# Kernel optimization log

Hardware: AMD Instinct MI355X
Metric: run time of the kernel (lower is better)

The kernel has to match this reference:

```python
import jax, jax.numpy as jnp
import numpy as np

N = 50000   # nodes
E = 500000  # edges
D = 128     # enc_dim == Hout
INIT_W = 0.1


def _lin_w(k, din, dout):
    return jax.random.normal(k, (dout, din), jnp.float32) * INIT_W


def setup_inputs() -> dict:
    key = jax.random.key(0)
    ks = jax.random.split(key, 16)
    inp = {
        "x": jax.random.normal(ks[0], (N, D), jnp.float32),
        "src": jax.random.randint(ks[1], (E,), 0, N),
        "dst": jax.random.randint(ks[2], (E,), 0, N),
        # encoders (Linear enc_dim -> enc_dim)
        "WencK": _lin_w(ks[3], D, D), "bencK": jnp.zeros((D,), jnp.float32),
        "WencP1": _lin_w(ks[4], D, D), "bencP1": jnp.zeros((D,), jnp.float32),
        "WencP2": _lin_w(ks[5], D, D), "bencP2": jnp.zeros((D,), jnp.float32),
        # Kfun: Linear-Tanh-Linear-ReLU-Linear
        "K0W": _lin_w(ks[6], D, D), "K0b": jnp.zeros((D,), jnp.float32),
        "K1W": _lin_w(ks[7], D, D), "K1b": jnp.zeros((D,), jnp.float32),
        "K2W": _lin_w(ks[8], D, D), "K2b": jnp.zeros((D,), jnp.float32),
        # Ufun: Linear-Tanh-Linear-ReLU-Linear
        "U0W": _lin_w(ks[9], D, D), "U0b": jnp.zeros((D,), jnp.float32),
        "U1W": _lin_w(ks[10], D, D), "U1b": jnp.zeros((D,), jnp.float32),
        "U2W": _lin_w(ks[11], D, D), "U2b": jnp.zeros((D,), jnp.float32),
    }
    return inp


def _mlp3(h, W0, b0, W1, b1, W2, b2):
    h = jnp.tanh(h @ W0.T + b0)
    h = jax.nn.relu(h @ W1.T + b1)
    return h @ W2.T + b2


def reference(x, src, dst,
              WencK, bencK, WencP1, bencP1, WencP2, bencP2,
              K0W, K0b, K1W, K1b, K2W, K2b,
              U0W, U0b, U1W, U1b, U2W, U2b):
    # getK: encode nodes, copy_u + sum to dst, node MLP
    h1 = x @ WencK.T + bencK                                   # [N, D]
    h1_agg = jax.ops.segment_sum(h1[src], dst, num_segments=N)  # [N, D]
    Knode = _mlp3(h1_agg, K0W, K0b, K1W, K1b, K2W, K2b)         # [N, D]
    # getU: u_add_v on encoded features, edge MLP
    p1 = x @ WencP1.T + bencP1
    p2 = x @ WencP2.T + bencP2
    Eedge = _mlp3(p1[src] + p2[dst], U0W, U0b, U1W, U1b, U2W, U2b)  # [E, D]
    # getH: u_mul_e + sum to dst
    Enew = jax.ops.segment_sum(Knode[src] * Eedge, dst, num_segments=N)  # [N, D]
    return jnp.sum(Enew)
```

## Files before the change

### kernel.cpp

```cpp
#include <hip/hip_runtime.h>
#include <hip/hip_bf16.h>
#include <math.h>

#define NN 50000
#define NE 500000
#define DD 128
#define STR 136
#define NSCAN (2 * NN)
#define SCAN_BLK ((NSCAN + 1023) / 1024)
#define HIST_BLK ((NE + 255) / 256)
#define CVT_BLK  ((NN * DD + 4095) / 4096)
#define PRECONV_BLK ((7 * 2048 + 1023) / 1024)
#define ENC_BLK  ((NN + 127) / 128)
#define TSCALE 2.885390081777927f

typedef __attribute__((ext_vector_type(8))) short short8;
typedef __attribute__((ext_vector_type(4))) float floatx4;

__device__ __forceinline__ float bf2f(unsigned short u) {
    unsigned v = ((unsigned)u) << 16;
    float f;
    __builtin_memcpy(&f, &v, 4);
    return f;
}
__device__ __forceinline__ unsigned short f2bf(float f) {
    unsigned x;
    __builtin_memcpy(&x, &f, 4);
    x += 0x7FFF + ((x >> 16) & 1);
    return (unsigned short)(x >> 16);
}
__device__ __forceinline__ float fast_tanh(float x) {
    float t = __builtin_amdgcn_exp2f(x * TSCALE);
    return 1.f - 2.f * __builtin_amdgcn_rcpf(t + 1.f);
}
__device__ __forceinline__ float fast_tanh_pre(float u) {
    float t = __builtin_amdgcn_exp2f(u);
    return 1.f - 2.f * __builtin_amdgcn_rcpf(t + 1.f);
}

__global__ __launch_bounds__(256) void k1_kernel(
    const int* __restrict__ src, const int* __restrict__ dst,
    int* __restrict__ cnt_dst, int* __restrict__ cnt_src,
    int* __restrict__ rank_d, int* __restrict__ rank_s,
    const float* __restrict__ x, unsigned short* __restrict__ xbf,
    const float* __restrict__ U0W, const float* __restrict__ WencP1,
    const float* __restrict__ WencP2, const float* __restrict__ K0W,
    const float* __restrict__ WencK,
    const float* __restrict__ bp1, const float* __restrict__ bp2,
    const float* __restrict__ U0b, const float* __restrict__ bk,
    const float* __restrict__ U2b,
    float* __restrict__ comp, float* __restrict__ bvecs)
{
    __shared__ float Bs[DD * DD];
    int blk = blockIdx.x;
    int t = threadIdx.x;

    if (blk < HIST_BLK) {
        int e = blk * 256 + t;
        if (e < NE) {
            rank_d[e] = atomicAdd(&cnt_dst[dst[e]], 1);
            rank_s[e] = atomicAdd(&cnt_src[src[e]], 1);
        }
        return;
    }
    if (blk < HIST_BLK + CVT_BLK) {
        int base = (blk - HIST_BLK) * 4096;
        #pragma unroll
        for (int j = 0; j < 4; ++j) {
            int idx = base + (j * 256 + t) * 4;
            if (idx < NN * DD) {
                float4 f = *(const float4*)&x[idx];
                ushort4 v4;
                v4.x = f2bf(f.x); v4.y = f2bf(f.y);
                v4.z = f2bf(f.z); v4.w = f2bf(f.w);
                *(ushort4*)&xbf[idx] = v4;
            }
        }
        return;
    }

    int b = blk - (HIST_BLK + CVT_BLK);
    if (b == 6) {
        if (t < 128) {
            float s1 = 0.f, s2 = 0.f;
            for (int k = 0; k < DD; ++k) {
                s1 += U0W[t * DD + k] * (bp1[k] + bp2[k]);
                s2 += K0W[t * DD + k] * bk[k];
            }
            bvecs[t] = (s1 + U0b[t]) * TSCALE;
            bvecs[128 + t] = s2;
            int f = (t & 64) + 16 * (t & 3) + ((t & 63) >> 2);
            bvecs[256 + t] = U2b[f];
        }
        return;
    }
    int mat = b >> 1, half = b & 1;
    const float* A = (mat == 2) ? K0W : U0W;
    const float* B = (mat == 0) ? WencP1 : (mat == 1) ? WencP2 : WencK;
    float scl = (mat == 2) ? 1.f : TSCALE;
    float* C = comp + (size_t)mat * DD * DD;
    for (int i = 0; i < 64; ++i)
        Bs[i * 256 + t] = B[i * 256 + t];
    __syncthreads();
    int row = half * 64 + (t >> 2);
    int j0 = (t & 3) * 32;
    float acc[32];
    #pragma unroll
    for (int jj = 0; jj < 32; ++jj) acc[jj] = 0.f;
    for (int k = 0; k < DD; ++k) {
        float a = A[row * DD + k];
        #pragma unroll
        for (int jj = 0; jj < 32; ++jj)
            acc[jj] += a * Bs[k * DD + j0 + jj];
    }
    #pragma unroll
    for (int jj = 0; jj < 32; ++jj) C[row * DD + j0 + jj] = acc[jj] * scl;
}

__global__ __launch_bounds__(1024) void k2_kernel(
    const float* __restrict__ comp, const float* __restrict__ K1W,
    const float* __restrict__ K2W, const float* __restrict__ U2W,
    const float* __restrict__ U1W, unsigned short* __restrict__ wfrag,
    const int* __restrict__ cnt, int* __restrict__ base, int* __restrict__ bsum)
{
    int t = threadIdx.x;
    if (blockIdx.x < PRECONV_BLK) {
        int g = blockIdx.x * 1024 + t;
        if (g >= 7 * 2048) return;
        int m = g >> 11;
        int rem = g & 2047;
        int kt = rem >> 9, nt = (rem >> 6) & 7, lane = rem & 63;
        const float* W;
        bool perm = false, tr = false;
        switch (m) {
            case 0: W = comp; break;
            case 1: W = comp + 16384; break;
            case 2: W = comp + 32768; break;
            case 3: W = K1W; perm = true; break;
            case 4: W = K2W; perm = true; break;
            case 5: W = U2W; perm = true; tr = true; break;
            default: W = U1W; break;
        }
        int n = nt * 16 + (lane & 15);
        #pragma unroll
        for (int j = 0; j < 8; ++j) {
            int ks = kt * 32 + (lane >> 4) * 8 + j;
            int f = perm ? (ks & 64) + 16 * (ks & 3) + ((ks & 63) >> 2) : ks;
            float v = tr ? W[f * DD + n] : W[n * DD + f];
            wfrag[(size_t)g * 8 + j] = f2bf(v);
        }
        return;
    }
    __shared__ int wsum[16];
    int sb = blockIdx.x - PRECONV_BLK;
    int i = sb * 1024 + t;
    int v = (i < NSCAN) ? cnt[i] : 0;
    int lane = t & 63, w = t >> 6;
    int xv = v;
    #pragma unroll
    for (int off = 1; off < 64; off <<= 1) {
        int y = __shfl_up(xv, off);
        if (lane >= off) xv += y;
    }
    if (lane == 63) wsum[w] = xv;
    __syncthreads();
    if (w == 0) {
        int s = (lane < 16) ? wsum[lane] : 0;
        #pragma unroll
        for (int off = 1; off < 16; off <<= 1) {
            int y = __shfl_up(s, off);
            if (lane >= off) s += y;
        }
        if (lane < 16) wsum[lane] = s;
    }
    __syncthreads();
    int wavebase = (w == 0) ? 0 : wsum[w - 1];
    int incl = wavebase + xv;
    if (i < NSCAN) base[i] = incl - v;
    if (t == 1023) bsum[sb] = incl;
}

__global__ __launch_bounds__(128) void scan2_kernel(
    int* __restrict__ bsum, float* __restrict__ out)
{
    if (threadIdx.x == 0 && blockIdx.x == 0) *out = 0.f;
    __shared__ int wsum[2];
    int t = threadIdx.x;
    int v = (t < SCAN_BLK) ? bsum[t] : 0;
    int lane = t & 63, w = t >> 6;
    int x = v;
    #pragma unroll
    for (int off = 1; off < 64; off <<= 1) {
        int y = __shfl_up(x, off);
        if (lane >= off) x += y;
    }
    if (lane == 63) wsum[w] = x;
    __syncthreads();
    int wavebase = (w == 0) ? 0 : wsum[0];
    int incl = wavebase + x;
    if (t < SCAN_BLK) bsum[t] = incl - v;
}

__global__ __launch_bounds__(256) void place_kernel(
    const int* __restrict__ src, const int* __restrict__ dst,
    const int* __restrict__ base, const int* __restrict__ bsum,
    const int* __restrict__ rank_d, const int* __restrict__ rank_s,
    int* __restrict__ sorted_src_bydst, int2* __restrict__ epairs)
{
    int e = blockIdx.x * 256 + threadIdx.x;
    if (e < NE) {
        int s = src[e], d = dst[e];
        sorted_src_bydst[base[d] + bsum[d >> 10] + rank_d[e]] = s;
        int si = NN + s;
        int p = base[si] + bsum[si >> 10] + rank_s[e] - NE;
        epairs[p] = make_int2(s, d);
    }
}

__global__ __launch_bounds__(256) void agg_kernel(
    const unsigned short* __restrict__ xbf,
    const int* __restrict__ base, const int* __restrict__ bsum,
    const int* __restrict__ cnt, const int* __restrict__ sorted_src,
    unsigned short* __restrict__ xagg)
{
    int node = blockIdx.x * 4 + (threadIdx.x >> 6);
    int lane = threadIdx.x & 63;
    if (node >= NN) return;
    int lo = base[node] + bsum[node >> 10];
    int hi = lo + cnt[node];
    const int rowg = lane >> 4;
    const int colc = lane & 15;
    float a[8];
    #pragma unroll
    for (int j = 0; j < 8; ++j) a[j] = 0.f;

    for (int off = lo; off < hi; off += 64) {
        int myid = (off + lane < hi) ? sorted_src[off + lane] : 0;
        int nk = min(64, hi - off);
        for (int k = 0; k < nk; k += 4) {
            int kk = k + rowg;
            int s = __shfl(myid, kk);
            if (kk < nk) {
                short8 v = *(const short8*)&xbf[(size_t)s * DD + colc * 8];
                #pragma unroll
                for (int j = 0; j < 8; ++j)
                    a[j] += bf2f((unsigned short)v[j]);
            }
        }
    }
    #pragma unroll
    for (int j = 0; j < 8; ++j) {
        a[j] += __shfl_xor(a[j], 16);
        a[j] += __shfl_xor(a[j], 32);
    }
    if (lane < 16) {
        short8 o;
        #pragma unroll
        for (int j = 0; j < 8; ++j) o[j] = (short)f2bf(a[j]);
        *(short8*)&xagg[(size_t)node * DD + lane * 8] = o;
    }
}

__global__ __launch_bounds__(256) void encnode_kernel(
    const unsigned short* __restrict__ xbf, const unsigned short* __restrict__ xagg,
    const unsigned short* __restrict__ wf, const float* __restrict__ bvecs,
    const int* __restrict__ cnt,
    const float* __restrict__ K0b, const float* __restrict__ K1b,
    const float* __restrict__ K2b,
    unsigned short* __restrict__ q1, unsigned short* __restrict__ q2,
    unsigned short* __restrict__ Km, float* __restrict__ kb)
{
    __shared__ unsigned short A[128 * STR];
    const int t = threadIdx.x;
    const int lane = t & 63, w = t >> 6;
    const int wm = w >> 1, wn = w & 1;
    const int c = lane & 15, q = lane >> 4;

    if (blockIdx.x < ENC_BLK) {
        const int row0 = blockIdx.x * 128;
        #pragma unroll
        for (int i = 0; i < 8; ++i) {
            int idx = i * 256 + t;
            int r = idx >> 4, ch = idx & 15;
            int gr = row0 + r;
            short8 v = (short8){0,0,0,0,0,0,0,0};
            if (gr < NN) v = *(const short8*)&xbf[(size_t)gr * DD + ch * 8];
            *(short8*)&A[r * STR + ch * 8] = v;
        }
        __syncthreads();

        for (int l = 0; l < 2; ++l) {
            floatx4 acc[4][4];
            #pragma unroll
            for (int i = 0; i < 4; ++i)
                #pragma unroll
                for (int j = 0; j < 4; ++j)
                    acc[i][j] = (floatx4){0.f, 0.f, 0.f, 0.f};
            const short8* W8 = (const short8*)(wf + (size_t)l * 16384);
            #pragma unroll
            for (int kt = 0; kt < 4; ++kt) {
                short8 af[4], bfr[4];
                #pragma unroll
                for (int i = 0; i < 4; ++i)
                    af[i] = *(const short8*)&A[(wm * 64 + i * 16 + c) * STR + kt * 32 + q * 8];
                #pragma unroll
                for (int j = 0; j < 4; ++j)
                    bfr[j] = W8[(kt * 8 + wn * 4 + j) * 64 + lane];
                #pragma unroll
                for (int i = 0; i < 4; ++i)
                    #pragma unroll
                    for (int j = 0; j < 4; ++j)
                        acc[i][j] = __builtin_amdgcn_mfma_f32_16x16x32_bf16(af[i], bfr[j], acc[i][j], 0, 0, 0);
            }
            unsigned short* pp = (l == 0) ? q1 : q2;
            float bv[4];
            #pragma unroll
            for (int j = 0; j < 4; ++j)
                bv[j] = (l == 0) ? bvecs[c + 16 * j + 64 * wn] : 0.f;

            #pragma unroll
            for (int i = 0; i < 4; ++i)
                #pragma unroll
                for (int r = 0; r < 4; ++r) {
                    int node = row0 + wm * 64 + i * 16 + 4 * q + r;
                    if (node < NN) {
                        #pragma unroll
                        for (int j = 0; j < 4; ++j)
                            pp[(size_t)node * DD + c + 16 * j + 64 * wn] = f2bf(acc[i][j][r] + bv[j]);
                    }
                }
        }
        return;
    }

    const int row0 = (blockIdx.x - ENC_BLK) * 128;
    #pragma unroll
    for (int i = 0; i < 8; ++i) {
        int idx = i * 256 + t;
        int r = idx >> 4, ch = idx & 15;
        int gr = row0 + r;
        short8 v = (short8){0,0,0,0,0,0,0,0};
        if (gr < NN) v = *(const short8*)&xagg[(size_t)gr * DD + ch * 8];
        *(short8*)&A[r * STR + ch * 8] = v;
    }
    __syncthreads();

    for (int l = 0; l < 4; ++l) {
        floatx4 acc[4][4];
        #pragma unroll
        for (int i = 0; i < 4; ++i)
            #pragma unroll
            for (int j = 0; j < 4; ++j)
                acc[i][j] = (floatx4){0.f, 0.f, 0.f, 0.f};
        const short8* W8 = (const short8*)(wf + (size_t)(2 + l) * 16384);
        #pragma unroll
        for (int kt = 0; kt < 4; ++kt) {
            short8 af[4], bfr[4];
            #pragma unroll
            for (int i = 0; i < 4; ++i)
                af[i] = *(const short8*)&A[(wm * 64 + i * 16 + c) * STR + kt * 32 + q * 8];
            #pragma unroll
            for (int j = 0; j < 4; ++j)
                bfr[j] = W8[(kt * 8 + wn * 4 + j) * 64 + lane];
            #pragma unroll
            for (int i = 0; i < 4; ++i)
                #pragma unroll
                for (int j = 0; j < 4; ++j)
                    acc[i][j] = __builtin_amdgcn_mfma_f32_16x16x32_bf16(af[i], bfr[j], acc[i][j], 0, 0, 0);
        }

        if (l < 3) {
            const float* bb = (l == 0) ? K0b : (l == 1) ? K1b : K2b;
            float bv[4];
            #pragma unroll
            for (int j = 0; j < 4; ++j) bv[j] = bb[c + 16 * j + 64 * wn];
            float bvv[4];
            #pragma unroll
            for (int j = 0; j < 4; ++j)
                bvv[j] = (l == 0) ? bvecs[128 + c + 16 * j + 64 * wn] : 0.f;

            __syncthreads();
            #pragma unroll
            for (int i = 0; i < 4; ++i)
                #pragma unroll
                for (int r = 0; r < 4; ++r) {
                    int node = row0 + wm * 64 + i * 16 + 4 * q + r;
                    float cn = (l == 0) ? (float)((node < NN) ? cnt[node] : 0) : 0.f;
                    float v0 = acc[i][0][r] + bv[0] + cn * bvv[0];
                    float v1 = acc[i][1][r] + bv[1] + cn * bvv[1];
                    float v2 = acc[i][2][r] + bv[2] + cn * bvv[2];
                    float v3 = acc[i][3][r] + bv[3] + cn * bvv[3];
                    if (l == 0) {
                        v0 = fast_tanh(v0); v1 = fast_tanh(v1);
                        v2 = fast_tanh(v2); v3 = fast_tanh(v3);
                    } else if (l == 1) {
                        v0 = fmaxf(v0, 0.f); v1 = fmaxf(v1, 0.f);
                        v2 = fmaxf(v2, 0.f); v3 = fmaxf(v3, 0.f);
                    }
                    ushort4 pk;
                    pk.x = f2bf(v0); pk.y = f2bf(v1); pk.z = f2bf(v2); pk.w = f2bf(v3);
                    int m = wm * 64 + i * 16 + 4 * q + r;
                    *(ushort4*)&A[m * STR + 4 * c + 64 * wn] = pk;
                }
            __syncthreads();

            if (l == 2) {
                if (t < 128) {
                    int node = row0 + t;
                    if (node < NN) {
                        float s = 0.f;
                        #pragma unroll
                        for (int ch = 0; ch < 16; ++ch) {
                            short8 v = *(const short8*)&A[t * STR + ch * 8];
                            #pragma unroll
                            for (int e = 0; e < 8; ++e)
                                s += bf2f((unsigned short)v[e]) * bvecs[256 + ch * 8 + e];
                        }
                        kb[node] = s;
                    }
                }
            }
        } else {
            #pragma unroll
            for (int i = 0; i < 4; ++i)
                #pragma unroll
                for (int r = 0; r < 4; ++r) {
                    int node = row0 + wm * 64 + i * 16 + 4 * q + r;
                    if (node < NN) {
                        ushort4 pk;
                        pk.x = f2bf(acc[i][0][r]);
                        pk.y = f2bf(acc[i][1][r]);
                        pk.z = f2bf(acc[i][2][r]);
                        pk.w = f2bf(acc[i][3][r]);
                        *(ushort4*)&Km[(size_t)node * DD + 4 * c + 64 * wn] = pk;
                    }
                }
        }
    }
}

__global__ __launch_bounds__(256) void edge_kernel(
    const unsigned short* __restrict__ q1, const unsigned short* __restrict__ q2,
    const unsigned short* __restrict__ Km, const float* __restrict__ kb,
    const int2* __restrict__ epairs,
    const unsigned short* __restrict__ wf, const float* __restrict__ U1b,
    float* __restrict__ out)
{
    __shared__ unsigned short A[128 * 128];
    const int t = threadIdx.x;
    const int lane = t & 63, w = t >> 6;
    const int wm = w >> 1, wn = w & 1;
    const int c = lane & 15, q = lane >> 4;
    const int e0 = blockIdx.x * 128;

    float part = 0.f;
    if (t < 128) {
        int e = e0 + t;
        if (e < NE) part += kb[epairs[e].x];
    }

    #pragma unroll
    for (int i = 0; i < 8; ++i) {
        int idx = i * 256 + t;
        int r = idx >> 4, ch = idx & 15;
        int e = e0 + r;
        int o32[4] = {0, 0, 0, 0};
        if (e < NE) {
            int2 p = epairs[e];
            short8 a8 = *(const short8*)&q1[(size_t)p.x * DD + ch * 8];
            short8 b8 = *(const short8*)&q2[(size_t)p.y * DD + ch * 8];
            #pragma unroll
            for (int k = 0; k < 8; k += 2) {
                float2 u;
                u.x = fast_tanh_pre(bf2f((unsigned short)a8[k])     + bf2f((unsigned short)b8[k]));
                u.y = fast_tanh_pre(bf2f((unsigned short)a8[k + 1]) + bf2f((unsigned short)b8[k + 1]));
                __hip_bfloat162 hb = __float22bfloat162_rn(u);
                __builtin_memcpy(&o32[k >> 1], &hb, 4);
            }
        }
        *(int4*)&A[r * 128 + (ch ^ (r & 15)) * 8] = *(int4*)o32;
    }
    __syncthreads();

    floatx4 acc[4][4];
    #pragma unroll
    for (int i = 0; i < 4; ++i)
        #pragma unroll
        for (int j = 0; j < 4; ++j)
            acc[i][j] = (floatx4){0.f, 0.f, 0.f, 0.f};
    const short8* W8 = (const short8*)(wf + (size_t)6 * 16384);
    #pragma unroll
    for (int kt = 0; kt < 4; ++kt) {
        short8 af[4], bfr[4];
        #pragma unroll
        for (int i = 0; i < 4; ++i)
            af[i] = *(const short8*)&A[(wm * 64 + i * 16 + c) * 128 + ((kt * 4 + q) ^ c) * 8];
        #pragma unroll
        for (int j = 0; j < 4; ++j)
            bfr[j] = W8[(kt * 8 + wn * 4 + j) * 64 + lane];
        #pragma unroll
        for (int i = 0; i < 4; ++i)
            #pragma unroll
            for (int j = 0; j < 4; ++j)
                acc[i][j] = __builtin_amdgcn_mfma_f32_16x16x32_bf16(af[i], bfr[j], acc[i][j], 0, 0, 0);
    }
    float bv[4];
    #pragma unroll
    for (int j = 0; j < 4; ++j) bv[j] = U1b[c + 16 * j + 64 * wn];

    const int* esrc = (const int*)epairs;
    #pragma unroll
    for (int i = 0; i < 4; ++i)
        #pragma unroll
        for (int r = 0; r < 4; ++r) {
            int m = wm * 64 + i * 16 + 4 * q + r;
            int e = e0 + m;
            if (e < NE) {
                int s = esrc[2 * e];
                ushort4 km4 = *(const ushort4*)&Km[(size_t)s * DD + 4 * c + 64 * wn];
                part += fmaxf(acc[i][0][r] + bv[0], 0.f) * bf2f(km4.x)
                      + fmaxf(acc[i][1][r] + bv[1], 0.f) * bf2f(km4.y)
                      + fmaxf(acc[i][2][r] + bv[2], 0.f) * bf2f(km4.z)
                      + fmaxf(acc[i][3][r] + bv[3], 0.f) * bf2f(km4.w);
            }
        }

    #pragma unroll
    for (int off = 32; off > 0; off >>= 1)
        part += __shfl_down(part, off);
    __syncthreads();
    float* red = (float*)A;
    if (lane == 0) red[w] = part;
    __syncthreads();
    if (t == 0)
        atomicAdd(out, red[0] + red[1] + red[2] + red[3]);
}

extern "C" void kernel_launch(void* const* d_in, const int* in_sizes, int n_in,
                              void* d_out, int out_size, void* d_ws, size_t ws_size,
                              hipStream_t stream)
{
    const float* x     = (const float*)d_in[0];
    const int*   src   = (const int*)  d_in[1];
    const int*   dst   = (const int*)  d_in[2];
    const float* WencK = (const float*)d_in[3];
    const float* bencK = (const float*)d_in[4];
    const float* WencP1= (const float*)d_in[5];
    const float* bencP1= (const float*)d_in[6];
    const float* WencP2= (const float*)d_in[7];
    const float* bencP2= (const float*)d_in[8];
    const float* K0W   = (const float*)d_in[9];
    const float* K0b   = (const float*)d_in[10];
    const float* K1W   = (const float*)d_in[11];
    const float* K1b   = (const float*)d_in[12];
    const float* K2W   = (const float*)d_in[13];
    const float* K2b   = (const float*)d_in[14];
    const float* U0W   = (const float*)d_in[15];
    const float* U0b   = (const float*)d_in[16];
    const float* U1W   = (const float*)d_in[17];
    const float* U1b   = (const float*)d_in[18];
    const float* U2W   = (const float*)d_in[19];
    const float* U2b   = (const float*)d_in[20];

    char* ws = (char*)d_ws;
    unsigned short* wfrag = (unsigned short*)ws;
    float* comp  = (float*)(ws + 0x40000);
    float* bvecs = (float*)(ws + 0x70000);
    unsigned short* xbf  = (unsigned short*)(ws + 0x71000);
    unsigned short* q1   = xbf + (size_t)NN * DD;
    unsigned short* q2   = q1 + (size_t)NN * DD;
    unsigned short* Kmg  = q2 + (size_t)NN * DD;
    unsigned short* xagg = Kmg + (size_t)NN * DD;
    float* kb       = (float*)(xagg + (size_t)NN * DD);
    int* cnt_dst    = (int*)(kb + NN);
    int* cnt_src    = cnt_dst + NN;
    int* base       = cnt_src + NN;
    int* bsum       = base + NSCAN;
    int* rank_d     = bsum + 128;
    int* rank_s     = rank_d + NE;
    int* sorted_src_bydst = rank_s + NE;
    int2* epairs    = (int2*)(sorted_src_bydst + NE);

    hipMemsetAsync(cnt_dst, 0, 2 * NN * sizeof(int), stream);

    k1_kernel<<<HIST_BLK + CVT_BLK + 7, 256, 0, stream>>>(
        src, dst, cnt_dst, cnt_src, rank_d, rank_s, x, xbf,
        U0W, WencP1, WencP2, K0W, WencK, bencP1, bencP2, U0b, bencK, U2b,
        comp, bvecs);

    k2_kernel<<<PRECONV_BLK + SCAN_BLK, 1024, 0, stream>>>(
        comp, K1W, K2W, U2W, U1W, wfrag, cnt_dst, base, bsum);

    scan2_kernel<<<1, 128, 0, stream>>>(bsum, (float*)d_out);

    place_kernel<<<HIST_BLK, 256, 0, stream>>>(
        src, dst, base, bsum, rank_d, rank_s, sorted_src_bydst, epairs);

    agg_kernel<<<(NN + 3) / 4, 256, 0, stream>>>(
        xbf, base, bsum, cnt_dst, sorted_src_bydst, xagg);

    encnode_kernel<<<2 * ENC_BLK, 256, 0, stream>>>(
        xbf, xagg, wfrag, bvecs, cnt_dst, K0b, K1b, K2b, q1, q2, Kmg, kb);

    edge_kernel<<<(NE + 127) / 128, 256, 0, stream>>>(
        q1, q2, Kmg, kb, epairs, wfrag, U1b, (float*)d_out);
}
```

Measured before the change: 334.4 us.

## Stage edge indices in shared memory, pad LDS tile instead of XOR swizzle, unfold tanh scale

The edge kernel now loads each block's src/dst edge pairs into shared memory once and reuses them for the gathers and the Km epilogue, instead of rereading epairs from global memory. The LDS A tile switches from an XOR swizzle to a padded row stride (STR = 136). The tanh prescale (2/ln2) is no longer folded into the composed weights and bias vector; it is applied inside fast_tanh, which adds one multiply per element. This adds a barrier and extra shared memory, and the padded layout may bring back bank conflicts.

```diff
diff --git a/kernel.cpp b/kernel.cpp
--- a/kernel.cpp
+++ b/kernel.cpp
@@ -12,7 +12,6 @@
 #define CVT_BLK  ((NN * DD + 4095) / 4096)
 #define PRECONV_BLK ((7 * 2048 + 1023) / 1024)
 #define ENC_BLK  ((NN + 127) / 128)
-#define TSCALE 2.885390081777927f
 
 typedef __attribute__((ext_vector_type(8))) short short8;
 typedef __attribute__((ext_vector_type(4))) float floatx4;
@@ -30,11 +29,7 @@
     return (unsigned short)(x >> 16);
 }
 __device__ __forceinline__ float fast_tanh(float x) {
-    float t = __builtin_amdgcn_exp2f(x * TSCALE);
-    return 1.f - 2.f * __builtin_amdgcn_rcpf(t + 1.f);
-}
-__device__ __forceinline__ float fast_tanh_pre(float u) {
-    float t = __builtin_amdgcn_exp2f(u);
+    float t = __builtin_amdgcn_exp2f(x * 2.88539008177793f);
     return 1.f - 2.f * __builtin_amdgcn_rcpf(t + 1.f);
 }
 
@@ -87,7 +82,7 @@
                 s1 += U0W[t * DD + k] * (bp1[k] + bp2[k]);
                 s2 += K0W[t * DD + k] * bk[k];
             }
-            bvecs[t] = (s1 + U0b[t]) * TSCALE;
+            bvecs[t] = s1 + U0b[t];
             bvecs[128 + t] = s2;
             int f = (t & 64) + 16 * (t & 3) + ((t & 63) >> 2);
             bvecs[256 + t] = U2b[f];
@@ -97,7 +92,6 @@
     int mat = b >> 1, half = b & 1;
     const float* A = (mat == 2) ? K0W : U0W;
     const float* B = (mat == 0) ? WencP1 : (mat == 1) ? WencP2 : WencK;
-    float scl = (mat == 2) ? 1.f : TSCALE;
     float* C = comp + (size_t)mat * DD * DD;
     for (int i = 0; i < 64; ++i)
         Bs[i * 256 + t] = B[i * 256 + t];
@@ -114,7 +108,7 @@
             acc[jj] += a * Bs[k * DD + j0 + jj];
     }
     #pragma unroll
-    for (int jj = 0; jj < 32; ++jj) C[row * DD + j0 + jj] = acc[jj] * scl;
+    for (int jj = 0; jj < 32; ++jj) C[row * DD + j0 + jj] = acc[jj];
 }
 
 __global__ __launch_bounds__(1024) void k2_kernel(
@@ -446,39 +440,51 @@
     const unsigned short* __restrict__ wf, const float* __restrict__ U1b,
     float* __restrict__ out)
 {
-    __shared__ unsigned short A[128 * 128];
+    __shared__ unsigned short A[128 * STR];
+    __shared__ int sidx[128];
+    __shared__ int didx[128];
+    __shared__ float red[4];
     const int t = threadIdx.x;
     const int lane = t & 63, w = t >> 6;
     const int wm = w >> 1, wn = w & 1;
     const int c = lane & 15, q = lane >> 4;
     const int e0 = blockIdx.x * 128;
 
-    float part = 0.f;
     if (t < 128) {
         int e = e0 + t;
-        if (e < NE) part += kb[epairs[e].x];
-    }
+        if (e < NE) {
+            int2 p = epairs[e];
+            sidx[t] = p.x;
+            didx[t] = p.y;
+        } else {
+            sidx[t] = -1;
+            didx[t] = 0;
+        }
+    }
+    __syncthreads();
+
+    float part = 0.f;
+    if (t < 128 && sidx[t] >= 0) part += kb[sidx[t]];
 
     #pragma unroll
     for (int i = 0; i < 8; ++i) {
         int idx = i * 256 + t;
         int r = idx >> 4, ch = idx & 15;
-        int e = e0 + r;
+        int s = sidx[r];
         int o32[4] = {0, 0, 0, 0};
-        if (e < NE) {
-            int2 p = epairs[e];
-            short8 a8 = *(const short8*)&q1[(size_t)p.x * DD + ch * 8];
-            short8 b8 = *(const short8*)&q2[(size_t)p.y * DD + ch * 8];
+        if (s >= 0) {
+            short8 a8 = *(const short8*)&q1[(size_t)s * DD + ch * 8];
+            short8 b8 = *(const short8*)&q2[(size_t)didx[r] * DD + ch * 8];
             #pragma unroll
             for (int k = 0; k < 8; k += 2) {
                 float2 u;
-                u.x = fast_tanh_pre(bf2f((unsigned short)a8[k])     + bf2f((unsigned short)b8[k]));
-                u.y = fast_tanh_pre(bf2f((unsigned short)a8[k + 1]) + bf2f((unsigned short)b8[k + 1]));
+                u.x = fast_tanh(bf2f((unsigned short)a8[k])     + bf2f((unsigned short)b8[k]));
+                u.y = fast_tanh(bf2f((unsigned short)a8[k + 1]) + bf2f((unsigned short)b8[k + 1]));
                 __hip_bfloat162 hb = __float22bfloat162_rn(u);
                 __builtin_memcpy(&o32[k >> 1], &hb, 4);
             }
         }
-        *(int4*)&A[r * 128 + (ch ^ (r & 15)) * 8] = *(int4*)o32;
+        *(int4*)&A[r * STR + ch * 8] = *(int4*)o32;
     }
     __syncthreads();
 
@@ -494,7 +500,7 @@
         short8 af[4], bfr[4];
         #pragma unroll
         for (int i = 0; i < 4; ++i)
-            af[i] = *(const short8*)&A[(wm * 64 + i * 16 + c) * 128 + ((kt * 4 + q) ^ c) * 8];
+            af[i] = *(const short8*)&A[(wm * 64 + i * 16 + c) * STR + kt * 32 + q * 8];
         #pragma unroll
         for (int j = 0; j < 4; ++j)
             bfr[j] = W8[(kt * 8 + wn * 4 + j) * 64 + lane];
@@ -508,15 +514,13 @@
     #pragma unroll
     for (int j = 0; j < 4; ++j) bv[j] = U1b[c + 16 * j + 64 * wn];
 
-    const int* esrc = (const int*)epairs;
     #pragma unroll
     for (int i = 0; i < 4; ++i)
         #pragma unroll
         for (int r = 0; r < 4; ++r) {
             int m = wm * 64 + i * 16 + 4 * q + r;
-            int e = e0 + m;
-            if (e < NE) {
-                int s = esrc[2 * e];
+            int s = sidx[m];
+            if (s >= 0) {
                 ushort4 km4 = *(const ushort4*)&Km[(size_t)s * DD + 4 * c + 64 * wn];
                 part += fmaxf(acc[i][0][r] + bv[0], 0.f) * bf2f(km4.x)
                       + fmaxf(acc[i][1][r] + bv[1], 0.f) * bf2f(km4.y)
@@ -528,8 +532,6 @@
     #pragma unroll
     for (int off = 32; off > 0; off >>= 1)
         part += __shfl_down(part, off);
-    __syncthreads();
-    float* red = (float*)A;
     if (lane == 0) red[w] = part;
     __syncthreads();
     if (t == 0)
```

After: 329.1 us. About the same (-1.6%).
